# Performance work log

Measured on AMD Instinct MI355X. Metric: run time of the kernel, lower is better.

The kernel has to match this reference:

```python
import jax, jax.numpy as jnp
import numpy as np

EPS = 1e-12  # torch F.normalize eps
TOP_K = 3    # hardcoded in DualPrompt eval path


def _l2norm(x, axis):
    n = jnp.sqrt(jnp.sum(x * x, axis=axis, keepdims=True))
    return x / jnp.maximum(n, EPS)


def setup_inputs() -> dict:
    key = jax.random.key(0)
    k1, k2, k3, k4, k5 = jax.random.split(key, 5)
    B, D = 1024, 768
    POOL, PLEN = 100, 8
    x_querry = jax.random.normal(k1, (B, D), dtype=jnp.float32)
    x_block = jax.random.normal(k2, (B, 197, D), dtype=jnp.float32)
    # tensor_prompt uses nn.init.uniform_ -> U[0,1)
    K = jax.random.uniform(k3, (POOL, D), dtype=jnp.float32)
    A = jax.random.uniform(k4, (POOL, D), dtype=jnp.float32)
    p = jax.random.uniform(k5, (PLEN, POOL, D), dtype=jnp.float32)
    return {"x_querry": x_querry, "x_block": x_block, "K": K, "A": A, "p": p, "l": 3}


def reference(x_querry, x_block, K, A, p, l):
    # l=3 is in e_layers; eval path (train=False, halfway=False)
    # a_querry: bd,kd->bkd  (attention-weighted query per pool entry)
    a_querry = x_querry[:, None, :] * jax.nn.softmax(A, axis=1)[None, :, :]  # [B,P,D]
    n_K = _l2norm(K, axis=1)            # [P,D]
    q = _l2norm(a_querry, axis=2)       # [B,P,D]
    aq_k = jnp.einsum('bkd,kd->bk', q, n_K)  # cosine sim [B,P]
    # top-k prompt selection (detached in original)
    _, k_idx = jax.lax.top_k(aq_k, TOP_K)    # [B,3]
    p_sel = p[:, k_idx]                      # [L,B,3,D]
    P_ = jnp.transpose(p_sel.sum(axis=2), (1, 0, 2))  # [B,L,D]
    i = p.shape[0] // 2                      # e_p_length // 2
    Ek = P_[:, :i, :]
    Ev = P_[:, i:, :]
    return Ek, Ev, x_block
```

## Files before the change

### kernel.cpp

```cpp
#include <hip/hip_runtime.h>
#include <hip/hip_bf16.h>

#define B_    1024
#define D_    768
#define POOL_ 100
#define KPAD  128
#define PLEN_ 8
#define TOPK_ 3
#define EK_ELEMS (B_ * 4 * D_)
#define XB_ELEMS (B_ * 197 * D_)
#define XB_F4    (XB_ELEMS / 4)

#define BT 8
#define SCORE_BLOCKS (B_ / BT)
#define THREADS 512
#define COPY_BLOCKS  4096
#define NBLOCKS (SCORE_BLOCKS + COPY_BLOCKS)

typedef float  f4_t __attribute__((ext_vector_type(4)));
typedef double d2_t __attribute__((ext_vector_type(2)));

__global__ void prep_kernel(const float* __restrict__ A, const float* __restrict__ K,
                            d2_t* __restrict__ W_T) {
    const int k = blockIdx.x;
    const int t = threadIdx.x;

    if (k >= POOL_) {
        for (int d = t; d < D_; d += 256)
            W_T[(size_t)d * KPAD + k] = d2_t{0.0, 0.0};
        return;
    }

    const int wave = t >> 6, lane = t & 63;
    __shared__ double red[4];

    double m = -1e300;
    for (int d = t; d < D_; d += 256) m = fmax(m, (double)A[k * D_ + d]);
    #pragma unroll
    for (int off = 32; off >= 1; off >>= 1) m = fmax(m, __shfl_xor(m, off));
    if (lane == 0) red[wave] = m;
    __syncthreads();
    m = fmax(fmax(red[0], red[1]), fmax(red[2], red[3]));
    __syncthreads();

    double s = 0.0;
    for (int d = t; d < D_; d += 256) s += exp((double)A[k * D_ + d] - m);
    #pragma unroll
    for (int off = 32; off >= 1; off >>= 1) s += __shfl_xor(s, off);
    if (lane == 0) red[wave] = s;
    __syncthreads();
    s = red[0] + red[1] + red[2] + red[3];
    __syncthreads();

    double ss = 0.0;
    for (int d = t; d < D_; d += 256) {
        double v = (double)K[k * D_ + d];
        ss += v * v;
    }
    #pragma unroll
    for (int off = 32; off >= 1; off >>= 1) ss += __shfl_xor(ss, off);
    if (lane == 0) red[wave] = ss;
    __syncthreads();
    ss = red[0] + red[1] + red[2] + red[3];
    const double n = fmax(sqrt(ss), 1e-12);

    for (int d = t; d < D_; d += 256) {
        const double smd = exp((double)A[k * D_ + d] - m) / s;
        W_T[(size_t)d * KPAD + k] = d2_t{smd * ((double)K[k * D_ + d] / n),
                                         smd * smd};
    }
}

__global__ void __launch_bounds__(THREADS)
fused_kernel(const float* __restrict__ xq,
             const d2_t* __restrict__ W_T,
             const float* __restrict__ p,
             const f4_t* __restrict__ xb,
             float* __restrict__ out) {
    const int t = threadIdx.x;

    if (blockIdx.x >= SCORE_BLOCKS) {
        f4_t* __restrict__ dst = (f4_t*)(out + 2 * (size_t)EK_ELEMS);
        size_t i = (size_t)(blockIdx.x - SCORE_BLOCKS) * THREADS + t;
        const size_t stride = (size_t)COPY_BLOCKS * THREADS;
        for (; i < (size_t)XB_F4; i += stride)
            dst[i] = xb[i];
        return;
    }

    __shared__ float  s_xqf[BT][D_];
    __shared__ d2_t   s_buf[BT][KPAD];
    __shared__ double s_aq[BT][KPAD];
    __shared__ int    s_idx[BT][TOPK_];

    const int b0    = blockIdx.x * BT;
    const int klane = t & (KPAD - 1);
    const int dq    = t >> 7;

    for (int i = t; i < BT * D_; i += THREADS)
        s_xqf[i / D_][i % D_] = xq[(size_t)(b0 + i / D_) * D_ + (i % D_)];
    __syncthreads();

    double dot[BT], sq[BT];
    #pragma unroll
    for (int bl = 0; bl < BT; ++bl) { dot[bl] = 0.0; sq[bl] = 0.0; }

    const int dbeg = dq * (D_ / 4);
    #pragma unroll 4
    for (int i = 0; i < D_ / 4; ++i) {
        const int d = dbeg + i;
        const d2_t w = W_T[(size_t)d * KPAD + klane];
        #pragma unroll
        for (int bl = 0; bl < BT; ++bl) {
            const double x = (double)s_xqf[bl][d];
            dot[bl] += x * w.x;
            sq[bl]  += (x * x) * w.y;
        }
    }

    #pragma unroll
    for (int r = 1; r < 4; ++r) {
        if (dq == r) {
            #pragma unroll
            for (int bl = 0; bl < BT; ++bl)
                s_buf[bl][klane] = d2_t{dot[bl], sq[bl]};
        }
        __syncthreads();
        if (dq == 0) {
            #pragma unroll
            for (int bl = 0; bl < BT; ++bl) {
                dot[bl] += s_buf[bl][klane].x;
                sq[bl]  += s_buf[bl][klane].y;
            }
        }
        __syncthreads();
    }
    if (dq == 0) {
        #pragma unroll
        for (int bl = 0; bl < BT; ++bl)
            s_aq[bl][klane] = dot[bl] / fmax(sqrt(sq[bl]), 1e-12);
    }
    __syncthreads();

    const int wave = t >> 6, lane = t & 63;
    if (wave < 4) {
        #pragma unroll
        for (int half = 0; half < 2; ++half) {
            const int bl = wave + half * 4;
            double v0 = s_aq[bl][lane];
            double v1 = (lane + 64 < POOL_) ? s_aq[bl][lane + 64] : -1e300;
            #pragma unroll
            for (int r = 0; r < TOPK_; ++r) {
                double v; int ki;
                if (v0 >= v1) { v = v0; ki = lane; }
                else          { v = v1; ki = lane + 64; }
                #pragma unroll
                for (int off = 32; off >= 1; off >>= 1) {
                    double ov = __shfl_xor(v, off);
                    int    oi = __shfl_xor(ki, off);
                    if (ov > v || (ov == v && oi < ki)) { v = ov; ki = oi; }
                }
                if (lane == 0) s_idx[bl][r] = ki;
                if (ki == lane)      v0 = -1e300;
                if (ki == lane + 64) v1 = -1e300;
            }
        }
    }
    __syncthreads();

    for (int w = t; w < BT * PLEN_ * 192; w += THREADS) {
        const int bl  = w / (PLEN_ * 192);
        const int rem = w % (PLEN_ * 192);
        const int j = rem / 192, c = rem % 192;
        const int i0 = s_idx[bl][0], i1 = s_idx[bl][1], i2 = s_idx[bl][2];
        const int b = b0 + bl;
        const f4_t* __restrict__ q0 = (const f4_t*)(p + (size_t)(j * POOL_ + i0) * D_);
        const f4_t* __restrict__ q1 = (const f4_t*)(p + (size_t)(j * POOL_ + i1) * D_);
        const f4_t* __restrict__ q2 = (const f4_t*)(p + (size_t)(j * POOL_ + i2) * D_);
        f4_t v = q0[c] + q1[c] + q2[c];
        float* dst = (j < 4) ? out + ((size_t)b * 4 + j) * D_
                             : out + EK_ELEMS + ((size_t)b * 4 + (j - 4)) * D_;
        ((f4_t*)dst)[c] = v;
    }
}

extern "C" void kernel_launch(void* const* d_in, const int* in_sizes, int n_in,
                              void* d_out, int out_size, void* d_ws, size_t ws_size,
                              hipStream_t stream) {
    const float* x_querry = (const float*)d_in[0];
    const float* x_block  = (const float*)d_in[1];
    const float* K        = (const float*)d_in[2];
    const float* A        = (const float*)d_in[3];
    const float* p        = (const float*)d_in[4];

    float* out = (float*)d_out;

    d2_t* W_T = (d2_t*)d_ws;

    prep_kernel<<<KPAD, 256, 0, stream>>>(A, K, W_T);
    fused_kernel<<<NBLOCKS, THREADS, 0, stream>>>(x_querry, W_T, p,
                                                  (const f4_t*)x_block, out);
}
```

Baseline: 247.1 us.

## Fold softmax/normalize prep into fused kernel with grid-level atomic counter handoff

Removes the separate prep kernel and has the first 100 score blocks compute the softmax-weighted normalized key table in-kernel. Every thread in those blocks releases an atomic increment, and all score blocks spin until the counter reaches the target before reading W_T. The intent is to hide the prep work and its launch behind the large x_block copy running in the other blocks. In exchange, a memset launch is added to reset the counter. The padding columns are no longer zeroed, and correctness relies on the low-index blocks all being co-resident.

```diff
diff --git a/kernel.cpp b/kernel.cpp
--- a/kernel.cpp
+++ b/kernel.cpp
@@ -16,67 +16,20 @@
 #define THREADS 512
 #define COPY_BLOCKS  4096
 #define NBLOCKS (SCORE_BLOCKS + COPY_BLOCKS)
+#define REL_TARGET (100u * 512u)
 
 typedef float  f4_t __attribute__((ext_vector_type(4)));
 typedef double d2_t __attribute__((ext_vector_type(2)));
 
-__global__ void prep_kernel(const float* __restrict__ A, const float* __restrict__ K,
-                            d2_t* __restrict__ W_T) {
-    const int k = blockIdx.x;
-    const int t = threadIdx.x;
-
-    if (k >= POOL_) {
-        for (int d = t; d < D_; d += 256)
-            W_T[(size_t)d * KPAD + k] = d2_t{0.0, 0.0};
-        return;
-    }
-
-    const int wave = t >> 6, lane = t & 63;
-    __shared__ double red[4];
-
-    double m = -1e300;
-    for (int d = t; d < D_; d += 256) m = fmax(m, (double)A[k * D_ + d]);
-    #pragma unroll
-    for (int off = 32; off >= 1; off >>= 1) m = fmax(m, __shfl_xor(m, off));
-    if (lane == 0) red[wave] = m;
-    __syncthreads();
-    m = fmax(fmax(red[0], red[1]), fmax(red[2], red[3]));
-    __syncthreads();
-
-    double s = 0.0;
-    for (int d = t; d < D_; d += 256) s += exp((double)A[k * D_ + d] - m);
-    #pragma unroll
-    for (int off = 32; off >= 1; off >>= 1) s += __shfl_xor(s, off);
-    if (lane == 0) red[wave] = s;
-    __syncthreads();
-    s = red[0] + red[1] + red[2] + red[3];
-    __syncthreads();
-
-    double ss = 0.0;
-    for (int d = t; d < D_; d += 256) {
-        double v = (double)K[k * D_ + d];
-        ss += v * v;
-    }
-    #pragma unroll
-    for (int off = 32; off >= 1; off >>= 1) ss += __shfl_xor(ss, off);
-    if (lane == 0) red[wave] = ss;
-    __syncthreads();
-    ss = red[0] + red[1] + red[2] + red[3];
-    const double n = fmax(sqrt(ss), 1e-12);
-
-    for (int d = t; d < D_; d += 256) {
-        const double smd = exp((double)A[k * D_ + d] - m) / s;
-        W_T[(size_t)d * KPAD + k] = d2_t{smd * ((double)K[k * D_ + d] / n),
-                                         smd * smd};
-    }
-}
-
 __global__ void __launch_bounds__(THREADS)
 fused_kernel(const float* __restrict__ xq,
-             const d2_t* __restrict__ W_T,
+             const float* __restrict__ A,
+             const float* __restrict__ K,
              const float* __restrict__ p,
              const f4_t* __restrict__ xb,
-             float* __restrict__ out) {
+             float* __restrict__ out,
+             d2_t* __restrict__ W_T,
+             unsigned int* __restrict__ ctr) {
     const int t = threadIdx.x;
 
     if (blockIdx.x >= SCORE_BLOCKS) {
@@ -92,6 +45,67 @@
     __shared__ d2_t   s_buf[BT][KPAD];
     __shared__ double s_aq[BT][KPAD];
     __shared__ int    s_idx[BT][TOPK_];
+    __shared__ double red8[8];
+
+    const int wave = t >> 6, lane = t & 63;
+
+    if (blockIdx.x < POOL_) {
+        const int k = blockIdx.x;
+
+        double m = -1e300;
+        for (int d = t; d < D_; d += THREADS) m = fmax(m, (double)A[k * D_ + d]);
+        #pragma unroll
+        for (int off = 32; off >= 1; off >>= 1) m = fmax(m, __shfl_xor(m, off));
+        if (lane == 0) red8[wave] = m;
+        __syncthreads();
+        {
+            double mm = red8[0];
+            #pragma unroll
+            for (int i = 1; i < 8; ++i) mm = fmax(mm, red8[i]);
+            m = mm;
+        }
+        __syncthreads();
+
+        double s = 0.0;
+        for (int d = t; d < D_; d += THREADS) s += exp((double)A[k * D_ + d] - m);
+        #pragma unroll
+        for (int off = 32; off >= 1; off >>= 1) s += __shfl_xor(s, off);
+        if (lane == 0) red8[wave] = s;
+        __syncthreads();
+        {
+            double ssum = 0.0;
+            #pragma unroll
+            for (int i = 0; i < 8; ++i) ssum += red8[i];
+            s = ssum;
+        }
+        __syncthreads();
+
+        double ss = 0.0;
+        for (int d = t; d < D_; d += THREADS) {
+            double v = (double)K[k * D_ + d];
+            ss += v * v;
+        }
+        #pragma unroll
+        for (int off = 32; off >= 1; off >>= 1) ss += __shfl_xor(ss, off);
+        if (lane == 0) red8[wave] = ss;
+        __syncthreads();
+        {
+            double sst = 0.0;
+            #pragma unroll
+            for (int i = 0; i < 8; ++i) sst += red8[i];
+            ss = sst;
+        }
+        const double n = fmax(sqrt(ss), 1e-12);
+
+        for (int d = t; d < D_; d += THREADS) {
+            const double smd = exp((double)A[k * D_ + d] - m) / s;
+            W_T[(size_t)d * KPAD + k] = d2_t{smd * ((double)K[k * D_ + d] / n),
+                                             smd * smd};
+        }
+        __hip_atomic_fetch_add(ctr, 1u, __ATOMIC_RELEASE,
+                               __HIP_MEMORY_SCOPE_AGENT);
+        __syncthreads();
+    }
 
     const int b0    = blockIdx.x * BT;
     const int klane = t & (KPAD - 1);
@@ -99,6 +113,14 @@
 
     for (int i = t; i < BT * D_; i += THREADS)
         s_xqf[i / D_][i % D_] = xq[(size_t)(b0 + i / D_) * D_ + (i % D_)];
+
+    if (t == 0) {
+        while (__hip_atomic_load(ctr, __ATOMIC_RELAXED,
+                                 __HIP_MEMORY_SCOPE_AGENT) < REL_TARGET)
+            __builtin_amdgcn_s_sleep(32);
+        (void)__hip_atomic_load(ctr, __ATOMIC_ACQUIRE,
+                                __HIP_MEMORY_SCOPE_AGENT);
+    }
     __syncthreads();
 
     double dot[BT], sq[BT];
@@ -142,7 +164,6 @@
     }
     __syncthreads();
 
-    const int wave = t >> 6, lane = t & 63;
     if (wave < 4) {
         #pragma unroll
         for (int half = 0; half < 2; ++half) {
@@ -196,8 +217,10 @@
     float* out = (float*)d_out;
 
     d2_t* W_T = (d2_t*)d_ws;
-
-    prep_kernel<<<KPAD, 256, 0, stream>>>(A, K, W_T);
-    fused_kernel<<<NBLOCKS, THREADS, 0, stream>>>(x_querry, W_T, p,
-                                                  (const f4_t*)x_block, out);
+    unsigned int* ctr = (unsigned int*)(W_T + (size_t)D_ * KPAD);
+
+    hipMemsetAsync(ctr, 0, sizeof(unsigned int), stream);
+    fused_kernel<<<NBLOCKS, THREADS, 0, stream>>>(x_querry, A, K, p,
+                                                  (const f4_t*)x_block, out,
+                                                  W_T, ctr);
 }
```

Measured after the change: 325.1 us. +31.5%, slower.
